# Kernel optimization log

Hardware: AMD Instinct MI355X
Metric: run time of the kernel (lower is better)

The kernel has to match this reference:

```python
import jax, jax.numpy as jnp
import numpy as np

D_MODEL = 1024
NHEAD = 16
D_K = D_MODEL // NHEAD
SPARSITY = 0.9
DROP_P = 0.1


def setup_inputs() -> dict:
    key = jax.random.key(0)
    ks = jax.random.split(key, 11)
    B, S = 4, 2048
    s = 1.0 / np.sqrt(D_MODEL)
    return {
        "query": jax.random.normal(ks[0], (B, S, D_MODEL), jnp.float32),
        "key": jax.random.normal(ks[1], (B, S, D_MODEL), jnp.float32),
        "value": jax.random.normal(ks[2], (B, S, D_MODEL), jnp.float32),
        "Wq": jax.random.normal(ks[3], (D_MODEL, D_MODEL), jnp.float32) * s,
        "bq": jnp.zeros((D_MODEL,), jnp.float32),
        "Wk": jax.random.normal(ks[4], (D_MODEL, D_MODEL), jnp.float32) * s,
        "bk": jnp.zeros((D_MODEL,), jnp.float32),
        "Wv": jax.random.normal(ks[5], (D_MODEL, D_MODEL), jnp.float32) * s,
        "bv": jnp.zeros((D_MODEL,), jnp.float32),
        "Wo": jax.random.normal(ks[6], (D_MODEL, D_MODEL), jnp.float32) * s,
        "bo": jnp.zeros((D_MODEL,), jnp.float32),
    }


def reference(query, key, value, Wq, bq, Wk, bk, Wv, bv, Wo, bo):
    B, S, _ = query.shape
    # torch Linear: x @ W.T + b
    def proj(x, W, b):
        return (x @ W.T + b).reshape(B, S, NHEAD, D_K).transpose(0, 2, 1, 3)

    Q = proj(query, Wq, bq)   # [B,H,S,d_k]
    K = proj(key, Wk, bk)
    V = proj(value, Wv, bv)

    scores = jnp.einsum("bhqd,bhkd->bhqk", Q, K) / jnp.sqrt(jnp.float32(D_K))
    # random sparsity mask: keep where rand > sparsity (fixed RNG key)
    mkey = jax.random.key(42)
    keep = jax.random.uniform(mkey, scores.shape, jnp.float32) > SPARSITY
    scores = jnp.where(keep, scores, -jnp.inf)
    probs = jax.nn.softmax(scores, axis=-1)
    # dropout on attention probs (train mode, inverted dropout)
    dkey = jax.random.key(7)
    dmask = jax.random.bernoulli(dkey, 1.0 - DROP_P, probs.shape)
    probs = probs * dmask / (1.0 - DROP_P)

    out = jnp.einsum("bhqk,bhkd->bhqd", probs, V)  # [B,H,S,d_k]
    out = out.transpose(0, 2, 1, 3).reshape(B, S, D_MODEL)
    return out @ Wo.T + bo
```

## Files before the change

### kernel.cpp

```cpp
#include <hip/hip_runtime.h>
#include <stdint.h>

typedef unsigned short u16;
typedef unsigned int u32;
typedef __attribute__((ext_vector_type(8))) short short8;
typedef __attribute__((ext_vector_type(4))) float f32x4;

#define DEVI static __device__ __forceinline__

#define S_LEN 2048
#define DMODEL 1024
#define NHEAD 16
#define DK 64
#define NEG_INF (-__builtin_inff())
#define KEEPC 3865470976u
#define DROPC 3865470464u

DEVI u16 f2bf(float f) {
  u32 u = __builtin_bit_cast(u32, f);
  u32 r = u + 0x7fffu + ((u >> 16) & 1u);
  return (u16)(r >> 16);
}

DEVI short8 cvt8(float4 a, float4 b) {
  short8 r;
  r[0] = (short)f2bf(a.x); r[1] = (short)f2bf(a.y);
  r[2] = (short)f2bf(a.z); r[3] = (short)f2bf(a.w);
  r[4] = (short)f2bf(b.x); r[5] = (short)f2bf(b.y);
  r[6] = (short)f2bf(b.z); r[7] = (short)f2bf(b.w);
  return r;
}

DEVI u32 tf_bits(u32 key, u32 i) {
  const u32 K2 = key ^ 0x1BD11BDAu;
  u32 x0 = 0u, x1 = i + key;
#define TFR(r) { x0 += x1; x1 = __builtin_rotateleft32(x1, r); x1 ^= x0; }
  TFR(13) TFR(15) TFR(26) TFR(6)  x0 += key; x1 += K2 + 1u;
  TFR(17) TFR(29) TFR(16) TFR(24) x0 += K2;  x1 += 2u;
  TFR(13) TFR(15) TFR(26) TFR(6)    x1 += key + 3u;
  TFR(17) TFR(29) TFR(16) TFR(24) x0 += key; x1 += K2 + 4u;
  TFR(13) TFR(15) TFR(26) TFR(6)  x0 += K2;  x1 += 5u;
#undef TFR
  return x0 ^ x1;
}

DEVI u32 keep16(u32 ib) {
  u32 m16 = 0;
  #pragma unroll
  for (int c = 0; c < 4; ++c) {
    #pragma unroll
    for (int r = 0; r < 4; ++r) {
      m16 |= (u32)(tf_bits(42u, ib + (u32)(r * 2048 + c * 16)) >= KEEPC) << (c * 4 + r);
    }
  }
  return m16;
}

DEVI u32 drop_balanced(u32 m16, u32 wb, int lane, u16* dwp) {
  const int cnt = __popc(m16);
  int pre = cnt;
  #pragma unroll
  for (int dlt = 1; dlt < 64; dlt <<= 1) {
    int t = __shfl_up(pre, dlt);
    if (lane >= dlt) pre += t;
  }
  const int total = __shfl(pre, 63);
  pre -= cnt;
  {
    u32 mm = m16; int jj = pre;
    while (mm) {
      const u32 s = (u32)__builtin_ctz(mm); mm &= mm - 1u;
      dwp[jj] = (u16)(((u32)lane << 4) | s);
      ++jj;
    }
  }
  for (int ws2 = lane; ws2 < total; ws2 += 64) {
    const u32 e = (u32)dwp[ws2];
    const u32 oo = e >> 4, ss = e & 15u;
    const u32 ii = wb + ((oo >> 4) * 4u + (ss & 3u)) * 2048u + (oo & 15u) + (ss >> 2) * 16u;
    dwp[ws2] = (u16)(e | ((u32)(tf_bits(7u, ii) < DROPC) << 15));
  }
  u32 d16 = 0;
  {
    u32 mm = m16; int jj = pre;
    while (mm) {
      const u32 s = (u32)__builtin_ctz(mm); mm &= mm - 1u;
      d16 |= (u32)((dwp[jj] >> 15) & 1u) << s;
      ++jj;
    }
  }
  return d16;
}

__global__ __launch_bounds__(256) void proj_kernel(
    const float* __restrict__ Xq, const float* __restrict__ Xk, const float* __restrict__ Xv,
    const float* __restrict__ Wq, const float* __restrict__ Wk, const float* __restrict__ Wv,
    const float* __restrict__ bq, const float* __restrict__ bk, const float* __restrict__ bv,
    u16* __restrict__ Qo, u16* __restrict__ Ko, u16* __restrict__ Vto)
{
  const int z = blockIdx.z;
  const float* X = (z == 0) ? Xq : (z == 1) ? Xk : Xv;
  const float* W = (z == 0) ? Wq : (z == 1) ? Wk : Wv;
  const float* bias = (z == 0) ? bq : (z == 1) ? bk : bv;
  const int m0 = blockIdx.x * 64, n0 = blockIdx.y * 64;
  const int tid = threadIdx.x, w = tid >> 6, lane = tid & 63, l = lane & 15, quad = lane >> 4;

  __shared__ __align__(16) u16 lsA[2048], lsB[2048];

  const int srow = tid >> 2, skp = tid & 3;
  const int sc = ((srow >> 4) * 64 + skp * 16 + (srow & 15)) * 8;
  const float* gA = X + (u32)(m0 + srow) * DMODEL + skp * 8;
  const float* gB = W + (u32)(n0 + srow) * DMODEL + skp * 8;

  f32x4 acc[2][2] = {};
  const int mh = (w >> 1) * 2, nh = (w & 1) * 2;

  for (int k0 = 0; k0 < DMODEL; k0 += 32) {
    short8 av  = cvt8(*(const float4*)(gA + k0), *(const float4*)(gA + k0 + 4));
    short8 bv8 = cvt8(*(const float4*)(gB + k0), *(const float4*)(gB + k0 + 4));
    __syncthreads();
    *(short8*)(lsA + sc) = av;
    *(short8*)(lsB + sc) = bv8;
    __syncthreads();
    short8 a0 = *(const short8*)(lsA + ((mh + 0) * 64 + lane) * 8);
    short8 a1 = *(const short8*)(lsA + ((mh + 1) * 64 + lane) * 8);
    short8 b0 = *(const short8*)(lsB + ((nh + 0) * 64 + lane) * 8);
    short8 b1 = *(const short8*)(lsB + ((nh + 1) * 64 + lane) * 8);
    acc[0][0] = __builtin_amdgcn_mfma_f32_16x16x32_bf16(a0, b0, acc[0][0], 0, 0, 0);
    acc[0][1] = __builtin_amdgcn_mfma_f32_16x16x32_bf16(a0, b1, acc[0][1], 0, 0, 0);
    acc[1][0] = __builtin_amdgcn_mfma_f32_16x16x32_bf16(a1, b0, acc[1][0], 0, 0, 0);
    acc[1][1] = __builtin_amdgcn_mfma_f32_16x16x32_bf16(a1, b1, acc[1][1], 0, 0, 0);
  }

  #pragma unroll
  for (int ma = 0; ma < 2; ++ma) {
    #pragma unroll
    for (int nb = 0; nb < 2; ++nb) {
      const int n = n0 + (nh + nb) * 16 + l;
      const float bval = bias[n];
      const int h = n >> 6, d = n & 63;
      #pragma unroll
      for (int r = 0; r < 4; ++r) {
        const int m = m0 + (mh + ma) * 16 + quad * 4 + r;
        float val = acc[ma][nb][r] + bval;
        if (z == 0) val *= 0.125f;
        const int b = m >> 11, s = m & 2047;
        if (z == 0)      Qo [((u32)(b * NHEAD + h) * S_LEN + s) * DK + d] = f2bf(val);
        else if (z == 1) Ko [((u32)(b * NHEAD + h) * S_LEN + s) * DK + d] = f2bf(val);
        else             Vto[((u32)(b * NHEAD + h) * DK + d) * S_LEN + s] = f2bf(val);
      }
    }
  }
}

__global__ __launch_bounds__(256) void attn_kernel(
    const u16* __restrict__ Qs, const u16* __restrict__ Ks, const u16* __restrict__ Vts,
    u16* __restrict__ ctx)
{
  const int qb = blockIdx.x, bh = blockIdx.y;
  const int tid = threadIdx.x, w = tid >> 6, lane = tid & 63, l = lane & 15, quad = lane >> 4;

  __shared__ __align__(16) u16 KPf[4096];
  __shared__ __align__(16) u16 Vf[4096];
  __shared__ __align__(16) u16 dbuf[1024];

  const int qrow0 = qb * 64 + w * 16;
  const u32 qbase = (u32)(bh * S_LEN + qrow0 + l) * DK + quad * 8;
  const short8 qa0 = *(const short8*)(Qs + qbase);
  const short8 qa1 = *(const short8*)(Qs + qbase + 32);

  u32 ibase = ((u32)bh * 2048u + (u32)(qrow0 + quad * 4)) * 2048u + (u32)l;
  const u32 wb0 = ((u32)bh * 2048u + (u32)qrow0) * 2048u;
  u16* const dwp = dbuf + w * 256;

  f32x4 o[4] = {};
  float mr[4] = {NEG_INF, NEG_INF, NEG_INF, NEG_INF};
  float lr[4] = {0.f, 0.f, 0.f, 0.f};

  const int kA  = ((tid >> 6) & 3) * 16 + (tid & 15);
  const int kdp = (tid >> 4) & 3;
  const u32 gk  = (u32)(bh * S_LEN + kA) * DK + kdp * 8;
  const int vd  = ((tid >> 7) & 1) * 16 + (tid & 15);
  const int vsp = ((tid >> 6) & 1) * 4 + ((tid >> 4) & 3);
  const u32 gvA = (u32)(bh * DK + vd) * S_LEN + vsp * 8;
  const u32 gvB = (u32)(bh * DK + vd + 32) * S_LEN + vsp * 8;

  const int hi = l >> 3, j = l & 7;
  const int pxor = ((quad >> 1) << 3) | (hi << 4);
  const int pb = (hi * 128 + quad * 32 + j) ^ pxor;
  const int prd = (lane * 8) ^ (lane & 24);
  u16* const pw = KPf + w * 1024;

  short8 k0v = *(const short8*)(Ks + gk);
  short8 k1v = *(const short8*)(Ks + gk + 32);
  short8 v0v = *(const short8*)(Vts + gvA);
  short8 v1v = *(const short8*)(Vts + gvB);
  u32 m16 = keep16(ibase);
  u32 d16 = drop_balanced(m16, wb0, lane, dwp);
  ibase += 64u;

  for (int kt = 0; kt < 32; ++kt) {
    __syncthreads();
    *(short8*)(KPf + tid * 8) = k0v;
    *(short8*)(KPf + 2048 + tid * 8) = k1v;
    *(short8*)(Vf + tid * 8) = v0v;
    *(short8*)(Vf + 2048 + tid * 8) = v1v;
    __syncthreads();

    {
      const u32 ko = (u32)(kt + 1) * 64u;
      k0v = *(const short8*)(Ks + gk + ko * DK);
      k1v = *(const short8*)(Ks + gk + ko * DK + 32);
      v0v = *(const short8*)(Vts + gvA + ko);
      v1v = *(const short8*)(Vts + gvB + ko);
    }

    f32x4 sc4[4];
    #pragma unroll
    for (int nc = 0; nc < 4; ++nc) {
      short8 kb0 = *(const short8*)(KPf + (nc * 64 + lane) * 8);
      short8 kb1 = *(const short8*)(KPf + ((4 + nc) * 64 + lane) * 8);
      f32x4 zz = {0.f, 0.f, 0.f, 0.f};
      zz = __builtin_amdgcn_mfma_f32_16x16x32_bf16(qa0, kb0, zz, 0, 0, 0);
      sc4[nc] = __builtin_amdgcn_mfma_f32_16x16x32_bf16(qa1, kb1, zz, 0, 0, 0);
    }
    const u32 m16n = keep16(ibase);

    __syncthreads();

    #pragma unroll
    for (int r = 0; r < 4; ++r) {
      float v0 = ((m16 >> (r + 0))  & 1u) ? sc4[0][r] : NEG_INF;
      float v1 = ((m16 >> (r + 4))  & 1u) ? sc4[1][r] : NEG_INF;
      float v2 = ((m16 >> (r + 8))  & 1u) ? sc4[2][r] : NEG_INF;
      float v3 = ((m16 >> (r + 12)) & 1u) ? sc4[3][r] : NEG_INF;
      float mx = fmaxf(fmaxf(v0, v1), fmaxf(v2, v3));
      mx = fmaxf(mx, __shfl_xor(mx, 1));
      mx = fmaxf(mx, __shfl_xor(mx, 2));
      mx = fmaxf(mx, __shfl_xor(mx, 4));
      mx = fmaxf(mx, __shfl_xor(mx, 8));
      const float mn = fmaxf(mr[r], mx);
      const float mnc = fmaxf(mn, -1e37f);
      const float alpha = __expf(mr[r] - mnc);
      mr[r] = mn;
      const float p0 = __expf(v0 - mnc);
      const float p1 = __expf(v1 - mnc);
      const float p2 = __expf(v2 - mnc);
      const float p3 = __expf(v3 - mnc);
      float rs = p0 + p1 + p2 + p3;
      rs += __shfl_xor(rs, 1);
      rs += __shfl_xor(rs, 2);
      rs += __shfl_xor(rs, 4);
      rs += __shfl_xor(rs, 8);
      lr[r] = alpha * lr[r] + rs;
      o[0][r] = o[0][r] * alpha; o[1][r] = o[1][r] * alpha;
      o[2][r] = o[2][r] * alpha; o[3][r] = o[3][r] * alpha;
      const float pd0 = ((d16 >> (r + 0))  & 1u) ? p0 * (1.f / 0.9f) : 0.f;
      const float pd1 = ((d16 >> (r + 4))  & 1u) ? p1 * (1.f / 0.9f) : 0.f;
      const float pd2 = ((d16 >> (r + 8))  & 1u) ? p2 * (1.f / 0.9f) : 0.f;
      const float pd3 = ((d16 >> (r + 12)) & 1u) ? p3 * (1.f / 0.9f) : 0.f;
      const int pi = pb ^ (r * 8);
      pw[pi      ] = f2bf(pd0);
      pw[pi + 256] = f2bf(pd1);
      pw[pi + 512] = f2bf(pd2);
      pw[pi + 768] = f2bf(pd3);
    }
    short8 pa0 = *(const short8*)(pw + prd);
    short8 pa1 = *(const short8*)(pw + 512 + prd);
    #pragma unroll
    for (int nd = 0; nd < 4; ++nd) {
      short8 vb0 = *(const short8*)(Vf + ((nd * 2 + 0) * 64 + lane) * 8);
      short8 vb1 = *(const short8*)(Vf + ((nd * 2 + 1) * 64 + lane) * 8);
      o[nd] = __builtin_amdgcn_mfma_f32_16x16x32_bf16(pa0, vb0, o[nd], 0, 0, 0);
      o[nd] = __builtin_amdgcn_mfma_f32_16x16x32_bf16(pa1, vb1, o[nd], 0, 0, 0);
    }

    u32 d16n = 0;
    if (kt < 31) d16n = drop_balanced(m16n, wb0 + (u32)(kt + 1) * 64u, lane, dwp);
    m16 = m16n; d16 = d16n;
    ibase += 64u;
  }

  const int b = bh >> 4, h = bh & 15;
  #pragma unroll
  for (int r = 0; r < 4; ++r) {
    const float inv = 1.f / lr[r];
    const int qrow = qb * 64 + w * 16 + quad * 4 + r;
    const u32 ob = (u32)(b * S_LEN + qrow) * DMODEL + h * DK;
    ctx[ob + 0  + l] = f2bf(o[0][r] * inv);
    ctx[ob + 16 + l] = f2bf(o[1][r] * inv);
    ctx[ob + 32 + l] = f2bf(o[2][r] * inv);
    ctx[ob + 48 + l] = f2bf(o[3][r] * inv);
  }
}

__global__ __launch_bounds__(256) void oproj_kernel(
    const u16* __restrict__ X, const float* __restrict__ W, const float* __restrict__ bias,
    float* __restrict__ out)
{
  const int m0 = blockIdx.x * 64, n0 = blockIdx.y * 64;
  const int tid = threadIdx.x, w = tid >> 6, lane = tid & 63, l = lane & 15, quad = lane >> 4;

  __shared__ __align__(16) u16 lsA[2048], lsB[2048];

  const int srow = tid >> 2, skp = tid & 3;
  const int sc = ((srow >> 4) * 64 + skp * 16 + (srow & 15)) * 8;
  const u16*  gA = X + (u32)(m0 + srow) * DMODEL + skp * 8;
  const float* gB = W + (u32)(n0 + srow) * DMODEL + skp * 8;

  f32x4 acc[2][2] = {};
  const int mh = (w >> 1) * 2, nh = (w & 1) * 2;

  for (int k0 = 0; k0 < DMODEL; k0 += 32) {
    short8 av  = *(const short8*)(gA + k0);
    short8 bv8 = cvt8(*(const float4*)(gB + k0), *(const float4*)(gB + k0 + 4));
    __syncthreads();
    *(short8*)(lsA + sc) = av;
    *(short8*)(lsB + sc) = bv8;
    __syncthreads();
    short8 a0 = *(const short8*)(lsA + ((mh + 0) * 64 + lane) * 8);
    short8 a1 = *(const short8*)(lsA + ((mh + 1) * 64 + lane) * 8);
    short8 b0 = *(const short8*)(lsB + ((nh + 0) * 64 + lane) * 8);
    short8 b1 = *(const short8*)(lsB + ((nh + 1) * 64 + lane) * 8);
    acc[0][0] = __builtin_amdgcn_mfma_f32_16x16x32_bf16(a0, b0, acc[0][0], 0, 0, 0);
    acc[0][1] = __builtin_amdgcn_mfma_f32_16x16x32_bf16(a0, b1, acc[0][1], 0, 0, 0);
    acc[1][0] = __builtin_amdgcn_mfma_f32_16x16x32_bf16(a1, b0, acc[1][0], 0, 0, 0);
    acc[1][1] = __builtin_amdgcn_mfma_f32_16x16x32_bf16(a1, b1, acc[1][1], 0, 0, 0);
  }

  #pragma unroll
  for (int ma = 0; ma < 2; ++ma) {
    #pragma unroll
    for (int nb = 0; nb < 2; ++nb) {
      const int n = n0 + (nh + nb) * 16 + l;
      const float bval = bias[n];
      #pragma unroll
      for (int r = 0; r < 4; ++r) {
        const int m = m0 + (mh + ma) * 16 + quad * 4 + r;
        out[(u32)m * DMODEL + n] = acc[ma][nb][r] + bval;
      }
    }
  }
}

extern "C" void kernel_launch(void* const* d_in, const int* in_sizes, int n_in,
                              void* d_out, int out_size, void* d_ws, size_t ws_size,
                              hipStream_t stream) {
  (void)in_sizes; (void)n_in; (void)out_size; (void)ws_size;
  const float* q  = (const float*)d_in[0];
  const float* k  = (const float*)d_in[1];
  const float* v  = (const float*)d_in[2];
  const float* Wq = (const float*)d_in[3];
  const float* bq = (const float*)d_in[4];
  const float* Wk = (const float*)d_in[5];
  const float* bk = (const float*)d_in[6];
  const float* Wv = (const float*)d_in[7];
  const float* bv = (const float*)d_in[8];
  const float* Wo = (const float*)d_in[9];
  const float* bo = (const float*)d_in[10];

  char* ws = (char*)d_ws;
  u16* Qs   = (u16*)(ws);
  u16* Ks   = (u16*)(ws + 16777216);
  u16* Vts  = (u16*)(ws + 33554432);
  u16* ctx  = (u16*)(ws + 50331648);

  proj_kernel<<<dim3(128, 16, 3), 256, 0, stream>>>(q, k, v, Wq, Wk, Wv,
                                                    bq, bk, bv, Qs, Ks, Vts);
  attn_kernel<<<dim3(32, 64), 256, 0, stream>>>(Qs, Ks, Vts, ctx);
  oproj_kernel<<<dim3(128, 16), 256, 0, stream>>>(ctx, Wo, bo, (float*)d_out);
}
```

Before: 1.109 ms.

## Restructure attention into single-wave blocks loading K/V fragments directly from global

The attention kernel moves from 4-wave blocks that stage K and V tiles through shared memory, with block barriers, to one-wave blocks over 16 query rows. Each wave loads its MFMA K and V operands straight from global memory and keeps only the P tile and dropout scratch in LDS. This removes the __syncthreads and the LDS staging cost. In exchange, K/V reuse drops fourfold and global/L2 traffic rises, and the software prefetch of the next tile is gone, so load latency is exposed.

Result: slower. 1.135 ms (+2.3%).

```diff
diff --git a/kernel.cpp b/kernel.cpp
--- a/kernel.cpp
+++ b/kernel.cpp
@@ -153,80 +153,75 @@
   }
 }
 
-__global__ __launch_bounds__(256) void attn_kernel(
+__global__ __launch_bounds__(64) void attn_kernel(
     const u16* __restrict__ Qs, const u16* __restrict__ Ks, const u16* __restrict__ Vts,
     u16* __restrict__ ctx)
 {
-  const int qb = blockIdx.x, bh = blockIdx.y;
-  const int tid = threadIdx.x, w = tid >> 6, lane = tid & 63, l = lane & 15, quad = lane >> 4;
-
-  __shared__ __align__(16) u16 KPf[4096];
-  __shared__ __align__(16) u16 Vf[4096];
-  __shared__ __align__(16) u16 dbuf[1024];
-
-  const int qrow0 = qb * 64 + w * 16;
+  const int bh = blockIdx.y;
+  const int lane = threadIdx.x;
+  const int l = lane & 15, quad = lane >> 4;
+  const int qrow0 = blockIdx.x * 16;
+
+  __shared__ __align__(16) u16 Pf[1024];
+  __shared__ __align__(16) u16 dwb[256];
+
   const u32 qbase = (u32)(bh * S_LEN + qrow0 + l) * DK + quad * 8;
   const short8 qa0 = *(const short8*)(Qs + qbase);
   const short8 qa1 = *(const short8*)(Qs + qbase + 32);
 
   u32 ibase = ((u32)bh * 2048u + (u32)(qrow0 + quad * 4)) * 2048u + (u32)l;
   const u32 wb0 = ((u32)bh * 2048u + (u32)qrow0) * 2048u;
-  u16* const dwp = dbuf + w * 256;
 
   f32x4 o[4] = {};
   float mr[4] = {NEG_INF, NEG_INF, NEG_INF, NEG_INF};
   float lr[4] = {0.f, 0.f, 0.f, 0.f};
 
-  const int kA  = ((tid >> 6) & 3) * 16 + (tid & 15);
-  const int kdp = (tid >> 4) & 3;
-  const u32 gk  = (u32)(bh * S_LEN + kA) * DK + kdp * 8;
-  const int vd  = ((tid >> 7) & 1) * 16 + (tid & 15);
-  const int vsp = ((tid >> 6) & 1) * 4 + ((tid >> 4) & 3);
-  const u32 gvA = (u32)(bh * DK + vd) * S_LEN + vsp * 8;
-  const u32 gvB = (u32)(bh * DK + vd + 32) * S_LEN + vsp * 8;
+  const u16* kfb = Ks  + (u32)bh * (S_LEN * DK) + (u32)l * DK + quad * 8;
+  const u16* vfb = Vts + (u32)bh * (DK * S_LEN) + (u32)l * S_LEN + quad * 8;
 
   const int hi = l >> 3, j = l & 7;
-  const int pxor = ((quad >> 1) << 3) | (hi << 4);
-  const int pb = (hi * 128 + quad * 32 + j) ^ pxor;
+  const int pb  = (hi * 128 + quad * 32 + j) ^ (((quad >> 1) << 3) | (hi << 4));
   const int prd = (lane * 8) ^ (lane & 24);
-  u16* const pw = KPf + w * 1024;
-
-  short8 k0v = *(const short8*)(Ks + gk);
-  short8 k1v = *(const short8*)(Ks + gk + 32);
-  short8 v0v = *(const short8*)(Vts + gvA);
-  short8 v1v = *(const short8*)(Vts + gvB);
-  u32 m16 = keep16(ibase);
-  u32 d16 = drop_balanced(m16, wb0, lane, dwp);
-  ibase += 64u;
 
   for (int kt = 0; kt < 32; ++kt) {
-    __syncthreads();
-    *(short8*)(KPf + tid * 8) = k0v;
-    *(short8*)(KPf + 2048 + tid * 8) = k1v;
-    *(short8*)(Vf + tid * 8) = v0v;
-    *(short8*)(Vf + 2048 + tid * 8) = v1v;
-    __syncthreads();
-
+    const u16* kbt = kfb + (u32)kt * (64 * DK);
+    short8 kf0 = *(const short8*)(kbt);
+    short8 kf1 = *(const short8*)(kbt + 1024);
+    short8 kf2 = *(const short8*)(kbt + 2048);
+    short8 kf3 = *(const short8*)(kbt + 3072);
+    short8 kg0 = *(const short8*)(kbt + 32);
+    short8 kg1 = *(const short8*)(kbt + 1056);
+    short8 kg2 = *(const short8*)(kbt + 2080);
+    short8 kg3 = *(const short8*)(kbt + 3104);
+
+    const u32 m16 = keep16(ibase);
+    ibase += 64u;
+
+    f32x4 sc4[4];
     {
-      const u32 ko = (u32)(kt + 1) * 64u;
-      k0v = *(const short8*)(Ks + gk + ko * DK);
-      k1v = *(const short8*)(Ks + gk + ko * DK + 32);
-      v0v = *(const short8*)(Vts + gvA + ko);
-      v1v = *(const short8*)(Vts + gvB + ko);
-    }
-
-    f32x4 sc4[4];
-    #pragma unroll
-    for (int nc = 0; nc < 4; ++nc) {
-      short8 kb0 = *(const short8*)(KPf + (nc * 64 + lane) * 8);
-      short8 kb1 = *(const short8*)(KPf + ((4 + nc) * 64 + lane) * 8);
       f32x4 zz = {0.f, 0.f, 0.f, 0.f};
-      zz = __builtin_amdgcn_mfma_f32_16x16x32_bf16(qa0, kb0, zz, 0, 0, 0);
-      sc4[nc] = __builtin_amdgcn_mfma_f32_16x16x32_bf16(qa1, kb1, zz, 0, 0, 0);
-    }
-    const u32 m16n = keep16(ibase);
-
-    __syncthreads();
+      zz = __builtin_amdgcn_mfma_f32_16x16x32_bf16(qa0, kf0, zz, 0, 0, 0);
+      sc4[0] = __builtin_amdgcn_mfma_f32_16x16x32_bf16(qa1, kg0, zz, 0, 0, 0);
+      zz = (f32x4){0.f, 0.f, 0.f, 0.f};
+      zz = __builtin_amdgcn_mfma_f32_16x16x32_bf16(qa0, kf1, zz, 0, 0, 0);
+      sc4[1] = __builtin_amdgcn_mfma_f32_16x16x32_bf16(qa1, kg1, zz, 0, 0, 0);
+      zz = (f32x4){0.f, 0.f, 0.f, 0.f};
+      zz = __builtin_amdgcn_mfma_f32_16x16x32_bf16(qa0, kf2, zz, 0, 0, 0);
+      sc4[2] = __builtin_amdgcn_mfma_f32_16x16x32_bf16(qa1, kg2, zz, 0, 0, 0);
+      zz = (f32x4){0.f, 0.f, 0.f, 0.f};
+      zz = __builtin_amdgcn_mfma_f32_16x16x32_bf16(qa0, kf3, zz, 0, 0, 0);
+      sc4[3] = __builtin_amdgcn_mfma_f32_16x16x32_bf16(qa1, kg3, zz, 0, 0, 0);
+    }
+
+    const u16* vbt = vfb + (u32)kt * 64u;
+    short8 vf[8];
+    #pragma unroll
+    for (int nd = 0; nd < 4; ++nd) {
+      vf[2 * nd]     = *(const short8*)(vbt + nd * (16 * S_LEN));
+      vf[2 * nd + 1] = *(const short8*)(vbt + nd * (16 * S_LEN) + 32);
+    }
+
+    const u32 d16 = drop_balanced(m16, wb0 + (u32)kt * 64u, lane, dwb);
 
     #pragma unroll
     for (int r = 0; r < 4; ++r) {
@@ -260,32 +255,25 @@
       const float pd2 = ((d16 >> (r + 8))  & 1u) ? p2 * (1.f / 0.9f) : 0.f;
       const float pd3 = ((d16 >> (r + 12)) & 1u) ? p3 * (1.f / 0.9f) : 0.f;
       const int pi = pb ^ (r * 8);
-      pw[pi      ] = f2bf(pd0);
-      pw[pi + 256] = f2bf(pd1);
-      pw[pi + 512] = f2bf(pd2);
-      pw[pi + 768] = f2bf(pd3);
-    }
-    short8 pa0 = *(const short8*)(pw + prd);
-    short8 pa1 = *(const short8*)(pw + 512 + prd);
+      Pf[pi      ] = f2bf(pd0);
+      Pf[pi + 256] = f2bf(pd1);
+      Pf[pi + 512] = f2bf(pd2);
+      Pf[pi + 768] = f2bf(pd3);
+    }
+    short8 pa0 = *(const short8*)(Pf + prd);
+    short8 pa1 = *(const short8*)(Pf + 512 + prd);
     #pragma unroll
     for (int nd = 0; nd < 4; ++nd) {
-      short8 vb0 = *(const short8*)(Vf + ((nd * 2 + 0) * 64 + lane) * 8);
-      short8 vb1 = *(const short8*)(Vf + ((nd * 2 + 1) * 64 + lane) * 8);
-      o[nd] = __builtin_amdgcn_mfma_f32_16x16x32_bf16(pa0, vb0, o[nd], 0, 0, 0);
-      o[nd] = __builtin_amdgcn_mfma_f32_16x16x32_bf16(pa1, vb1, o[nd], 0, 0, 0);
-    }
-
-    u32 d16n = 0;
-    if (kt < 31) d16n = drop_balanced(m16n, wb0 + (u32)(kt + 1) * 64u, lane, dwp);
-    m16 = m16n; d16 = d16n;
-    ibase += 64u;
+      o[nd] = __builtin_amdgcn_mfma_f32_16x16x32_bf16(pa0, vf[2 * nd],     o[nd], 0, 0, 0);
+      o[nd] = __builtin_amdgcn_mfma_f32_16x16x32_bf16(pa1, vf[2 * nd + 1], o[nd], 0, 0, 0);
+    }
   }
 
   const int b = bh >> 4, h = bh & 15;
   #pragma unroll
   for (int r = 0; r < 4; ++r) {
     const float inv = 1.f / lr[r];
-    const int qrow = qb * 64 + w * 16 + quad * 4 + r;
+    const int qrow = qrow0 + quad * 4 + r;
     const u32 ob = (u32)(b * S_LEN + qrow) * DMODEL + h * DK;
     ctx[ob + 0  + l] = f2bf(o[0][r] * inv);
     ctx[ob + 16 + l] = f2bf(o[1][r] * inv);
@@ -367,6 +355,6 @@
 
   proj_kernel<<<dim3(128, 16, 3), 256, 0, stream>>>(q, k, v, Wq, Wk, Wv,
                                                     bq, bk, bv, Qs, Ks, Vts);
-  attn_kernel<<<dim3(32, 64), 256, 0, stream>>>(Qs, Ks, Vts, ctx);
+  attn_kernel<<<dim3(128, 64), 64, 0, stream>>>(Qs, Ks, Vts, ctx);
   oproj_kernel<<<dim3(128, 16), 256, 0, stream>>>(ctx, Wo, bo, (float*)d_out);
 }
```

## Split mask RNG generation into a separate kernel and load packed masks in attention

Applied to the files above, without the earlier changes.

Adds a maskgen kernel that computes the keep and dropout bitmasks for every 16x64 tile and writes them to workspace as packed u32 words. The attention kernel then loads one word per lane per key tile instead of running the RNG and the LDS-based dropout balancing inline. The old inline-RNG path is kept as a fallback when the workspace is smaller than 128 MB. This trades 64 MB of extra global writes and reads for less ALU and LDS work inside the attention loop. Which path runs depends on the workspace size the harness provides.

Measured after the change: 1.148 ms. 1.03x slower.

```diff
diff --git a/kernel.cpp b/kernel.cpp
--- a/kernel.cpp
+++ b/kernel.cpp
@@ -153,25 +153,35 @@
   }
 }
 
-__global__ __launch_bounds__(256) void attn_kernel(
+__global__ __launch_bounds__(256) void maskgen_kernel(u32* __restrict__ Mout) {
+  const int tid = threadIdx.x, w = tid >> 6, lane = tid & 63;
+  const int l = lane & 15, quad = lane >> 4;
+  __shared__ u16 dbuf[1024];
+
+  const u32 gw = (u32)blockIdx.x * 4u + (u32)w;
+  const u32 kt = gw & 31u, qt = (gw >> 5) & 127u, bh = gw >> 12;
+  const u32 ibase = (bh * 2048u + qt * 16u + (u32)quad * 4u) * 2048u + kt * 64u + (u32)l;
+  const u32 wb    = (bh * 2048u + qt * 16u) * 2048u + kt * 64u;
+
+  const u32 m16 = keep16(ibase);
+  const u32 d16 = drop_balanced(m16, wb, lane, dbuf + w * 256);
+  Mout[gw * 64u + (u32)lane] = m16 | (d16 << 16);
+}
+
+__global__ __launch_bounds__(256) void attn_pre_kernel(
     const u16* __restrict__ Qs, const u16* __restrict__ Ks, const u16* __restrict__ Vts,
-    u16* __restrict__ ctx)
+    const u32* __restrict__ Mask, u16* __restrict__ ctx)
 {
   const int qb = blockIdx.x, bh = blockIdx.y;
   const int tid = threadIdx.x, w = tid >> 6, lane = tid & 63, l = lane & 15, quad = lane >> 4;
 
   __shared__ __align__(16) u16 KPf[4096];
   __shared__ __align__(16) u16 Vf[4096];
-  __shared__ __align__(16) u16 dbuf[1024];
 
   const int qrow0 = qb * 64 + w * 16;
   const u32 qbase = (u32)(bh * S_LEN + qrow0 + l) * DK + quad * 8;
   const short8 qa0 = *(const short8*)(Qs + qbase);
   const short8 qa1 = *(const short8*)(Qs + qbase + 32);
-
-  u32 ibase = ((u32)bh * 2048u + (u32)(qrow0 + quad * 4)) * 2048u + (u32)l;
-  const u32 wb0 = ((u32)bh * 2048u + (u32)qrow0) * 2048u;
-  u16* const dwp = dbuf + w * 256;
 
   f32x4 o[4] = {};
   float mr[4] = {NEG_INF, NEG_INF, NEG_INF, NEG_INF};
@@ -185,9 +195,10 @@
   const u32 gvA = (u32)(bh * DK + vd) * S_LEN + vsp * 8;
   const u32 gvB = (u32)(bh * DK + vd + 32) * S_LEN + vsp * 8;
 
+  const u32* mb = Mask + ((u32)(bh * 128 + qb * 4 + w) * 32u) * 64u + (u32)lane;
+
   const int hi = l >> 3, j = l & 7;
-  const int pxor = ((quad >> 1) << 3) | (hi << 4);
-  const int pb = (hi * 128 + quad * 32 + j) ^ pxor;
+  const int pb  = (hi * 128 + quad * 32 + j) ^ (((quad >> 1) << 3) | (hi << 4));
   const int prd = (lane * 8) ^ (lane & 24);
   u16* const pw = KPf + w * 1024;
 
@@ -195,9 +206,7 @@
   short8 k1v = *(const short8*)(Ks + gk + 32);
   short8 v0v = *(const short8*)(Vts + gvA);
   short8 v1v = *(const short8*)(Vts + gvB);
-  u32 m16 = keep16(ibase);
-  u32 d16 = drop_balanced(m16, wb0, lane, dwp);
-  ibase += 64u;
+  u32 md = mb[0];
 
   for (int kt = 0; kt < 32; ++kt) {
     __syncthreads();
@@ -214,6 +223,7 @@
       v0v = *(const short8*)(Vts + gvA + ko);
       v1v = *(const short8*)(Vts + gvB + ko);
     }
+    const u32 mdn = mb[(u32)((kt + 1) & 31) * 64u];
 
     f32x4 sc4[4];
     #pragma unroll
@@ -224,10 +234,10 @@
       zz = __builtin_amdgcn_mfma_f32_16x16x32_bf16(qa0, kb0, zz, 0, 0, 0);
       sc4[nc] = __builtin_amdgcn_mfma_f32_16x16x32_bf16(qa1, kb1, zz, 0, 0, 0);
     }
-    const u32 m16n = keep16(ibase);
-
-    __syncthreads();
-
+
+    __syncthreads();
+
+    const u32 m16 = md & 0xffffu, d16 = md >> 16;
     #pragma unroll
     for (int r = 0; r < 4; ++r) {
       float v0 = ((m16 >> (r + 0))  & 1u) ? sc4[0][r] : NEG_INF;
@@ -274,11 +284,7 @@
       o[nd] = __builtin_amdgcn_mfma_f32_16x16x32_bf16(pa0, vb0, o[nd], 0, 0, 0);
       o[nd] = __builtin_amdgcn_mfma_f32_16x16x32_bf16(pa1, vb1, o[nd], 0, 0, 0);
     }
-
-    u32 d16n = 0;
-    if (kt < 31) d16n = drop_balanced(m16n, wb0 + (u32)(kt + 1) * 64u, lane, dwp);
-    m16 = m16n; d16 = d16n;
-    ibase += 64u;
+    md = mdn;
   }
 
   const int b = bh >> 4, h = bh & 15;
@@ -294,6 +300,147 @@
   }
 }
 
+__global__ __launch_bounds__(256) void attn_rng_kernel(
+    const u16* __restrict__ Qs, const u16* __restrict__ Ks, const u16* __restrict__ Vts,
+    u16* __restrict__ ctx)
+{
+  const int qb = blockIdx.x, bh = blockIdx.y;
+  const int tid = threadIdx.x, w = tid >> 6, lane = tid & 63, l = lane & 15, quad = lane >> 4;
+
+  __shared__ __align__(16) u16 KPf[4096];
+  __shared__ __align__(16) u16 Vf[4096];
+  __shared__ __align__(16) u16 dbuf[1024];
+
+  const int qrow0 = qb * 64 + w * 16;
+  const u32 qbase = (u32)(bh * S_LEN + qrow0 + l) * DK + quad * 8;
+  const short8 qa0 = *(const short8*)(Qs + qbase);
+  const short8 qa1 = *(const short8*)(Qs + qbase + 32);
+
+  u32 ibase = ((u32)bh * 2048u + (u32)(qrow0 + quad * 4)) * 2048u + (u32)l;
+  const u32 wb0 = ((u32)bh * 2048u + (u32)qrow0) * 2048u;
+  u16* const dwp = dbuf + w * 256;
+
+  f32x4 o[4] = {};
+  float mr[4] = {NEG_INF, NEG_INF, NEG_INF, NEG_INF};
+  float lr[4] = {0.f, 0.f, 0.f, 0.f};
+
+  const int kA  = ((tid >> 6) & 3) * 16 + (tid & 15);
+  const int kdp = (tid >> 4) & 3;
+  const u32 gk  = (u32)(bh * S_LEN + kA) * DK + kdp * 8;
+  const int vd  = ((tid >> 7) & 1) * 16 + (tid & 15);
+  const int vsp = ((tid >> 6) & 1) * 4 + ((tid >> 4) & 3);
+  const u32 gvA = (u32)(bh * DK + vd) * S_LEN + vsp * 8;
+  const u32 gvB = (u32)(bh * DK + vd + 32) * S_LEN + vsp * 8;
+
+  const int hi = l >> 3, j = l & 7;
+  const int pxor = ((quad >> 1) << 3) | (hi << 4);
+  const int pb = (hi * 128 + quad * 32 + j) ^ pxor;
+  const int prd = (lane * 8) ^ (lane & 24);
+  u16* const pw = KPf + w * 1024;
+
+  short8 k0v = *(const short8*)(Ks + gk);
+  short8 k1v = *(const short8*)(Ks + gk + 32);
+  short8 v0v = *(const short8*)(Vts + gvA);
+  short8 v1v = *(const short8*)(Vts + gvB);
+  u32 m16 = keep16(ibase);
+  u32 d16 = drop_balanced(m16, wb0, lane, dwp);
+  ibase += 64u;
+
+  for (int kt = 0; kt < 32; ++kt) {
+    __syncthreads();
+    *(short8*)(KPf + tid * 8) = k0v;
+    *(short8*)(KPf + 2048 + tid * 8) = k1v;
+    *(short8*)(Vf + tid * 8) = v0v;
+    *(short8*)(Vf + 2048 + tid * 8) = v1v;
+    __syncthreads();
+
+    {
+      const u32 ko = (u32)(kt + 1) * 64u;
+      k0v = *(const short8*)(Ks + gk + ko * DK);
+      k1v = *(const short8*)(Ks + gk + ko * DK + 32);
+      v0v = *(const short8*)(Vts + gvA + ko);
+      v1v = *(const short8*)(Vts + gvB + ko);
+    }
+
+    f32x4 sc4[4];
+    #pragma unroll
+    for (int nc = 0; nc < 4; ++nc) {
+      short8 kb0 = *(const short8*)(KPf + (nc * 64 + lane) * 8);
+      short8 kb1 = *(const short8*)(KPf + ((4 + nc) * 64 + lane) * 8);
+      f32x4 zz = {0.f, 0.f, 0.f, 0.f};
+      zz = __builtin_amdgcn_mfma_f32_16x16x32_bf16(qa0, kb0, zz, 0, 0, 0);
+      sc4[nc] = __builtin_amdgcn_mfma_f32_16x16x32_bf16(qa1, kb1, zz, 0, 0, 0);
+    }
+    const u32 m16n = keep16(ibase);
+
+    __syncthreads();
+
+    #pragma unroll
+    for (int r = 0; r < 4; ++r) {
+      float v0 = ((m16 >> (r + 0))  & 1u) ? sc4[0][r] : NEG_INF;
+      float v1 = ((m16 >> (r + 4))  & 1u) ? sc4[1][r] : NEG_INF;
+      float v2 = ((m16 >> (r + 8))  & 1u) ? sc4[2][r] : NEG_INF;
+      float v3 = ((m16 >> (r + 12)) & 1u) ? sc4[3][r] : NEG_INF;
+      float mx = fmaxf(fmaxf(v0, v1), fmaxf(v2, v3));
+      mx = fmaxf(mx, __shfl_xor(mx, 1));
+      mx = fmaxf(mx, __shfl_xor(mx, 2));
+      mx = fmaxf(mx, __shfl_xor(mx, 4));
+      mx = fmaxf(mx, __shfl_xor(mx, 8));
+      const float mn = fmaxf(mr[r], mx);
+      const float mnc = fmaxf(mn, -1e37f);
+      const float alpha = __expf(mr[r] - mnc);
+      mr[r] = mn;
+      const float p0 = __expf(v0 - mnc);
+      const float p1 = __expf(v1 - mnc);
+      const float p2 = __expf(v2 - mnc);
+      const float p3 = __expf(v3 - mnc);
+      float rs = p0 + p1 + p2 + p3;
+      rs += __shfl_xor(rs, 1);
+      rs += __shfl_xor(rs, 2);
+      rs += __shfl_xor(rs, 4);
+      rs += __shfl_xor(rs, 8);
+      lr[r] = alpha * lr[r] + rs;
+      o[0][r] = o[0][r] * alpha; o[1][r] = o[1][r] * alpha;
+      o[2][r] = o[2][r] * alpha; o[3][r] = o[3][r] * alpha;
+      const float pd0 = ((d16 >> (r + 0))  & 1u) ? p0 * (1.f / 0.9f) : 0.f;
+      const float pd1 = ((d16 >> (r + 4))  & 1u) ? p1 * (1.f / 0.9f) : 0.f;
+      const float pd2 = ((d16 >> (r + 8))  & 1u) ? p2 * (1.f / 0.9f) : 0.f;
+      const float pd3 = ((d16 >> (r + 12)) & 1u) ? p3 * (1.f / 0.9f) : 0.f;
+      const int pi = pb ^ (r * 8);
+      pw[pi      ] = f2bf(pd0);
+      pw[pi + 256] = f2bf(pd1);
+      pw[pi + 512] = f2bf(pd2);
+      pw[pi + 768] = f2bf(pd3);
+    }
+    short8 pa0 = *(const short8*)(pw + prd);
+    short8 pa1 = *(const short8*)(pw + 512 + prd);
+    #pragma unroll
+    for (int nd = 0; nd < 4; ++nd) {
+      short8 vb0 = *(const short8*)(Vf + ((nd * 2 + 0) * 64 + lane) * 8);
+      short8 vb1 = *(const short8*)(Vf + ((nd * 2 + 1) * 64 + lane) * 8);
+      o[nd] = __builtin_amdgcn_mfma_f32_16x16x32_bf16(pa0, vb0, o[nd], 0, 0, 0);
+      o[nd] = __builtin_amdgcn_mfma_f32_16x16x32_bf16(pa1, vb1, o[nd], 0, 0, 0);
+    }
+
+    u32 d16n = 0;
+    if (kt < 31) d16n = drop_balanced(m16n, wb0 + (u32)(kt + 1) * 64u, lane, dwp);
+    m16 = m16n; d16 = d16n;
+    ibase += 64u;
+  }
+
+  const int b = bh >> 4, h = bh & 15;
+  #pragma unroll
+  for (int r = 0; r < 4; ++r) {
+    const float inv = 1.f / lr[r];
+    const int qrow = qb * 64 + w * 16 + quad * 4 + r;
+    const u32 ob = (u32)(b * S_LEN + qrow) * DMODEL + h * DK;
+    ctx[ob + 0  + l] = f2bf(o[0][r] * inv);
+    ctx[ob + 16 + l] = f2bf(o[1][r] * inv);
+    ctx[ob + 32 + l] = f2bf(o[2][r] * inv);
+    ctx[ob + 48 + l] = f2bf(o[3][r] * inv);
+  }
+}
+
 __global__ __launch_bounds__(256) void oproj_kernel(
     const u16* __restrict__ X, const float* __restrict__ W, const float* __restrict__ bias,
     float* __restrict__ out)
@@ -346,7 +493,7 @@
 extern "C" void kernel_launch(void* const* d_in, const int* in_sizes, int n_in,
                               void* d_out, int out_size, void* d_ws, size_t ws_size,
                               hipStream_t stream) {
-  (void)in_sizes; (void)n_in; (void)out_size; (void)ws_size;
+  (void)in_sizes; (void)n_in; (void)out_size;
   const float* q  = (const float*)d_in[0];
   const float* k  = (const float*)d_in[1];
   const float* v  = (const float*)d_in[2];
@@ -364,9 +511,15 @@
   u16* Ks   = (u16*)(ws + 16777216);
   u16* Vts  = (u16*)(ws + 33554432);
   u16* ctx  = (u16*)(ws + 50331648);
+  u32* Mask = (u32*)(ws + 67108864);
 
   proj_kernel<<<dim3(128, 16, 3), 256, 0, stream>>>(q, k, v, Wq, Wk, Wv,
                                                     bq, bk, bv, Qs, Ks, Vts);
-  attn_kernel<<<dim3(32, 64), 256, 0, stream>>>(Qs, Ks, Vts, ctx);
+  if (ws_size >= (size_t)134217728) {
+    maskgen_kernel<<<65536, 256, 0, stream>>>(Mask);
+    attn_pre_kernel<<<dim3(32, 64), 256, 0, stream>>>(Qs, Ks, Vts, Mask, ctx);
+  } else {
+    attn_rng_kernel<<<dim3(32, 64), 256, 0, stream>>>(Qs, Ks, Vts, ctx);
+  }
   oproj_kernel<<<dim3(128, 16), 256, 0, stream>>>(ctx, Wo, bo, (float*)d_out);
 }
```

## Pre-convert inputs and weights to bf16 and double the GEMM K-step

Applied to the files above, without the earlier changes.

Adds a separate conversion kernel that turns the fp32 activations and all four weight matrices into bf16 once. The projection GEMMs then read bf16 directly instead of re-reading and re-converting fp32 tiles for every output tile. The GEMM K-loop now stages 64 elements per iteration with larger shared buffers, which halves the number of barriers. This costs an extra launch and an extra pass over the inputs (a read plus a bf16 write), and uses more LDS per block.

Result: faster. 1.067 ms (-3.8%).

```diff
diff --git a/kernel.cpp b/kernel.cpp
--- a/kernel.cpp
+++ b/kernel.cpp
@@ -92,44 +92,80 @@
   return d16;
 }
 
+__global__ __launch_bounds__(256) void cvt_kernel(
+    const float* __restrict__ xq, const float* __restrict__ xk, const float* __restrict__ xv,
+    const float* __restrict__ wq, const float* __restrict__ wk, const float* __restrict__ wv,
+    const float* __restrict__ wo,
+    u16* __restrict__ dxq, u16* __restrict__ dxk, u16* __restrict__ dxv,
+    u16* __restrict__ dwq, u16* __restrict__ dwk, u16* __restrict__ dwv,
+    u16* __restrict__ dwo)
+{
+  const int z = blockIdx.y;
+  const float* s; u16* d; u32 n;
+  switch (z) {
+    case 0:  s = xq; d = dxq; n = 8388608u; break;
+    case 1:  s = xk; d = dxk; n = 8388608u; break;
+    case 2:  s = xv; d = dxv; n = 8388608u; break;
+    case 3:  s = wq; d = dwq; n = 1048576u; break;
+    case 4:  s = wk; d = dwk; n = 1048576u; break;
+    case 5:  s = wv; d = dwv; n = 1048576u; break;
+    default: s = wo; d = dwo; n = 1048576u; break;
+  }
+  const u32 i = ((u32)blockIdx.x * 256u + (u32)threadIdx.x) * 8u;
+  if (i >= n) return;
+  *(short8*)(d + i) = cvt8(*(const float4*)(s + i), *(const float4*)(s + i + 4));
+}
+
 __global__ __launch_bounds__(256) void proj_kernel(
-    const float* __restrict__ Xq, const float* __restrict__ Xk, const float* __restrict__ Xv,
-    const float* __restrict__ Wq, const float* __restrict__ Wk, const float* __restrict__ Wv,
+    const u16* __restrict__ Xq, const u16* __restrict__ Xk, const u16* __restrict__ Xv,
+    const u16* __restrict__ Wq, const u16* __restrict__ Wk, const u16* __restrict__ Wv,
     const float* __restrict__ bq, const float* __restrict__ bk, const float* __restrict__ bv,
     u16* __restrict__ Qo, u16* __restrict__ Ko, u16* __restrict__ Vto)
 {
   const int z = blockIdx.z;
-  const float* X = (z == 0) ? Xq : (z == 1) ? Xk : Xv;
-  const float* W = (z == 0) ? Wq : (z == 1) ? Wk : Wv;
+  const u16* X = (z == 0) ? Xq : (z == 1) ? Xk : Xv;
+  const u16* W = (z == 0) ? Wq : (z == 1) ? Wk : Wv;
   const float* bias = (z == 0) ? bq : (z == 1) ? bk : bv;
   const int m0 = blockIdx.x * 64, n0 = blockIdx.y * 64;
   const int tid = threadIdx.x, w = tid >> 6, lane = tid & 63, l = lane & 15, quad = lane >> 4;
 
-  __shared__ __align__(16) u16 lsA[2048], lsB[2048];
+  __shared__ __align__(16) u16 lsA[8192], lsB[8192];
 
   const int srow = tid >> 2, skp = tid & 3;
   const int sc = ((srow >> 4) * 64 + skp * 16 + (srow & 15)) * 8;
-  const float* gA = X + (u32)(m0 + srow) * DMODEL + skp * 8;
-  const float* gB = W + (u32)(n0 + srow) * DMODEL + skp * 8;
+  const u16* gA = X + (u32)(m0 + srow) * DMODEL + skp * 8;
+  const u16* gB = W + (u32)(n0 + srow) * DMODEL + skp * 8;
 
   f32x4 acc[2][2] = {};
   const int mh = (w >> 1) * 2, nh = (w & 1) * 2;
 
-  for (int k0 = 0; k0 < DMODEL; k0 += 32) {
-    short8 av  = cvt8(*(const float4*)(gA + k0), *(const float4*)(gA + k0 + 4));
-    short8 bv8 = cvt8(*(const float4*)(gB + k0), *(const float4*)(gB + k0 + 4));
-    __syncthreads();
-    *(short8*)(lsA + sc) = av;
-    *(short8*)(lsB + sc) = bv8;
-    __syncthreads();
-    short8 a0 = *(const short8*)(lsA + ((mh + 0) * 64 + lane) * 8);
-    short8 a1 = *(const short8*)(lsA + ((mh + 1) * 64 + lane) * 8);
-    short8 b0 = *(const short8*)(lsB + ((nh + 0) * 64 + lane) * 8);
-    short8 b1 = *(const short8*)(lsB + ((nh + 1) * 64 + lane) * 8);
-    acc[0][0] = __builtin_amdgcn_mfma_f32_16x16x32_bf16(a0, b0, acc[0][0], 0, 0, 0);
-    acc[0][1] = __builtin_amdgcn_mfma_f32_16x16x32_bf16(a0, b1, acc[0][1], 0, 0, 0);
-    acc[1][0] = __builtin_amdgcn_mfma_f32_16x16x32_bf16(a1, b0, acc[1][0], 0, 0, 0);
-    acc[1][1] = __builtin_amdgcn_mfma_f32_16x16x32_bf16(a1, b1, acc[1][1], 0, 0, 0);
+  for (int k0 = 0; k0 < DMODEL; k0 += 64) {
+    short8 a0v = *(const short8*)(gA + k0);
+    short8 a1v = *(const short8*)(gA + k0 + 32);
+    short8 b0v = *(const short8*)(gB + k0);
+    short8 b1v = *(const short8*)(gB + k0 + 32);
+    __syncthreads();
+    *(short8*)(lsA + sc) = a0v;
+    *(short8*)(lsA + 4096 + sc) = a1v;
+    *(short8*)(lsB + sc) = b0v;
+    *(short8*)(lsB + 4096 + sc) = b1v;
+    __syncthreads();
+    short8 A00 = *(const short8*)(lsA + ((mh + 0) * 64 + lane) * 8);
+    short8 A10 = *(const short8*)(lsA + ((mh + 1) * 64 + lane) * 8);
+    short8 B00 = *(const short8*)(lsB + ((nh + 0) * 64 + lane) * 8);
+    short8 B10 = *(const short8*)(lsB + ((nh + 1) * 64 + lane) * 8);
+    acc[0][0] = __builtin_amdgcn_mfma_f32_16x16x32_bf16(A00, B00, acc[0][0], 0, 0, 0);
+    acc[0][1] = __builtin_amdgcn_mfma_f32_16x16x32_bf16(A00, B10, acc[0][1], 0, 0, 0);
+    acc[1][0] = __builtin_amdgcn_mfma_f32_16x16x32_bf16(A10, B00, acc[1][0], 0, 0, 0);
+    acc[1][1] = __builtin_amdgcn_mfma_f32_16x16x32_bf16(A10, B10, acc[1][1], 0, 0, 0);
+    short8 A01 = *(const short8*)(lsA + 4096 + ((mh + 0) * 64 + lane) * 8);
+    short8 A11 = *(const short8*)(lsA + 4096 + ((mh + 1) * 64 + lane) * 8);
+    short8 B01 = *(const short8*)(lsB + 4096 + ((nh + 0) * 64 + lane) * 8);
+    short8 B11 = *(const short8*)(lsB + 4096 + ((nh + 1) * 64 + lane) * 8);
+    acc[0][0] = __builtin_amdgcn_mfma_f32_16x16x32_bf16(A01, B01, acc[0][0], 0, 0, 0);
+    acc[0][1] = __builtin_amdgcn_mfma_f32_16x16x32_bf16(A01, B11, acc[0][1], 0, 0, 0);
+    acc[1][0] = __builtin_amdgcn_mfma_f32_16x16x32_bf16(A11, B01, acc[1][0], 0, 0, 0);
+    acc[1][1] = __builtin_amdgcn_mfma_f32_16x16x32_bf16(A11, B11, acc[1][1], 0, 0, 0);
   }
 
   #pragma unroll
@@ -295,37 +331,49 @@
 }
 
 __global__ __launch_bounds__(256) void oproj_kernel(
-    const u16* __restrict__ X, const float* __restrict__ W, const float* __restrict__ bias,
+    const u16* __restrict__ X, const u16* __restrict__ W, const float* __restrict__ bias,
     float* __restrict__ out)
 {
   const int m0 = blockIdx.x * 64, n0 = blockIdx.y * 64;
   const int tid = threadIdx.x, w = tid >> 6, lane = tid & 63, l = lane & 15, quad = lane >> 4;
 
-  __shared__ __align__(16) u16 lsA[2048], lsB[2048];
+  __shared__ __align__(16) u16 lsA[8192], lsB[8192];
 
   const int srow = tid >> 2, skp = tid & 3;
   const int sc = ((srow >> 4) * 64 + skp * 16 + (srow & 15)) * 8;
-  const u16*  gA = X + (u32)(m0 + srow) * DMODEL + skp * 8;
-  const float* gB = W + (u32)(n0 + srow) * DMODEL + skp * 8;
+  const u16* gA = X + (u32)(m0 + srow) * DMODEL + skp * 8;
+  const u16* gB = W + (u32)(n0 + srow) * DMODEL + skp * 8;
 
   f32x4 acc[2][2] = {};
   const int mh = (w >> 1) * 2, nh = (w & 1) * 2;
 
-  for (int k0 = 0; k0 < DMODEL; k0 += 32) {
-    short8 av  = *(const short8*)(gA + k0);
-    short8 bv8 = cvt8(*(const float4*)(gB + k0), *(const float4*)(gB + k0 + 4));
-    __syncthreads();
-    *(short8*)(lsA + sc) = av;
-    *(short8*)(lsB + sc) = bv8;
-    __syncthreads();
-    short8 a0 = *(const short8*)(lsA + ((mh + 0) * 64 + lane) * 8);
-    short8 a1 = *(const short8*)(lsA + ((mh + 1) * 64 + lane) * 8);
-    short8 b0 = *(const short8*)(lsB + ((nh + 0) * 64 + lane) * 8);
-    short8 b1 = *(const short8*)(lsB + ((nh + 1) * 64 + lane) * 8);
-    acc[0][0] = __builtin_amdgcn_mfma_f32_16x16x32_bf16(a0, b0, acc[0][0], 0, 0, 0);
-    acc[0][1] = __builtin_amdgcn_mfma_f32_16x16x32_bf16(a0, b1, acc[0][1], 0, 0, 0);
-    acc[1][0] = __builtin_amdgcn_mfma_f32_16x16x32_bf16(a1, b0, acc[1][0], 0, 0, 0);
-    acc[1][1] = __builtin_amdgcn_mfma_f32_16x16x32_bf16(a1, b1, acc[1][1], 0, 0, 0);
+  for (int k0 = 0; k0 < DMODEL; k0 += 64) {
+    short8 a0v = *(const short8*)(gA + k0);
+    short8 a1v = *(const short8*)(gA + k0 + 32);
+    short8 b0v = *(const short8*)(gB + k0);
+    short8 b1v = *(const short8*)(gB + k0 + 32);
+    __syncthreads();
+    *(short8*)(lsA + sc) = a0v;
+    *(short8*)(lsA + 4096 + sc) = a1v;
+    *(short8*)(lsB + sc) = b0v;
+    *(short8*)(lsB + 4096 + sc) = b1v;
+    __syncthreads();
+    short8 A00 = *(const short8*)(lsA + ((mh + 0) * 64 + lane) * 8);
+    short8 A10 = *(const short8*)(lsA + ((mh + 1) * 64 + lane) * 8);
+    short8 B00 = *(const short8*)(lsB + ((nh + 0) * 64 + lane) * 8);
+    short8 B10 = *(const short8*)(lsB + ((nh + 1) * 64 + lane) * 8);
+    acc[0][0] = __builtin_amdgcn_mfma_f32_16x16x32_bf16(A00, B00, acc[0][0], 0, 0, 0);
+    acc[0][1] = __builtin_amdgcn_mfma_f32_16x16x32_bf16(A00, B10, acc[0][1], 0, 0, 0);
+    acc[1][0] = __builtin_amdgcn_mfma_f32_16x16x32_bf16(A10, B00, acc[1][0], 0, 0, 0);
+    acc[1][1] = __builtin_amdgcn_mfma_f32_16x16x32_bf16(A10, B10, acc[1][1], 0, 0, 0);
+    short8 A01 = *(const short8*)(lsA + 4096 + ((mh + 0) * 64 + lane) * 8);
+    short8 A11 = *(const short8*)(lsA + 4096 + ((mh + 1) * 64 + lane) * 8);
+    short8 B01 = *(const short8*)(lsB + 4096 + ((nh + 0) * 64 + lane) * 8);
+    short8 B11 = *(const short8*)(lsB + 4096 + ((nh + 1) * 64 + lane) * 8);
+    acc[0][0] = __builtin_amdgcn_mfma_f32_16x16x32_bf16(A01, B01, acc[0][0], 0, 0, 0);
+    acc[0][1] = __builtin_amdgcn_mfma_f32_16x16x32_bf16(A01, B11, acc[0][1], 0, 0, 0);
+    acc[1][0] = __builtin_amdgcn_mfma_f32_16x16x32_bf16(A11, B01, acc[1][0], 0, 0, 0);
+    acc[1][1] = __builtin_amdgcn_mfma_f32_16x16x32_bf16(A11, B11, acc[1][1], 0, 0, 0);
   }
 
   #pragma unroll
@@ -364,9 +412,18 @@
   u16* Ks   = (u16*)(ws + 16777216);
   u16* Vts  = (u16*)(ws + 33554432);
   u16* ctx  = (u16*)(ws + 50331648);
-
-  proj_kernel<<<dim3(128, 16, 3), 256, 0, stream>>>(q, k, v, Wq, Wk, Wv,
+  u16* Xqb  = (u16*)(ws + 67108864);
+  u16* Xkb  = (u16*)(ws + 83886080);
+  u16* Xvb  = (u16*)(ws + 100663296);
+  u16* Wqb  = (u16*)(ws + 117440512);
+  u16* Wkb  = (u16*)(ws + 119537664);
+  u16* Wvb  = (u16*)(ws + 121634816);
+  u16* Wob  = (u16*)(ws + 123731968);
+
+  cvt_kernel<<<dim3(4096, 7), 256, 0, stream>>>(q, k, v, Wq, Wk, Wv, Wo,
+                                                Xqb, Xkb, Xvb, Wqb, Wkb, Wvb, Wob);
+  proj_kernel<<<dim3(128, 16, 3), 256, 0, stream>>>(Xqb, Xkb, Xvb, Wqb, Wkb, Wvb,
                                                     bq, bk, bv, Qs, Ks, Vts);
   attn_kernel<<<dim3(32, 64), 256, 0, stream>>>(Qs, Ks, Vts, ctx);
-  oproj_kernel<<<dim3(128, 16), 256, 0, stream>>>(ctx, Wo, bo, (float*)d_out);
-}
+  oproj_kernel<<<dim3(128, 16), 256, 0, stream>>>(ctx, Wob, bo, (float*)d_out);
+}
```
